# Optimization experiments

Hardware: AMD Instinct MI355X
Metric: run time of the kernel (lower is better)

## Reference

```python
import jax, jax.numpy as jnp
import numpy as np

N = 100000
E = 1600000
D = 128


def setup_inputs() -> dict:
    key = jax.random.key(0)
    ks = jax.random.split(key, 8)
    x = jax.random.normal(ks[0], (N, D), dtype=jnp.float32)
    edge_index = jax.random.randint(ks[1], (2, E), 0, N, dtype=jnp.int64)
    # Xavier-uniform linear weights, zero-ish biases (PyTorch default bias is uniform; keep small random)
    def xavier(k, fan_in, fan_out):
        limit = float(np.sqrt(6.0 / (fan_in + fan_out)))
        return jax.random.uniform(k, (fan_out, fan_in), minval=-limit, maxval=limit, dtype=jnp.float32)
    W1 = xavier(ks[2], D, D); b1 = jnp.zeros((D,), jnp.float32)
    W2 = xavier(ks[3], D, D); b2 = jnp.zeros((D,), jnp.float32)
    W3 = xavier(ks[4], D, D); b3 = jnp.zeros((D,), jnp.float32)
    return {"x": x, "edge_index": edge_index, "W1": W1, "b1": b1,
            "W2": W2, "b2": b2, "W3": W3, "b3": b3}


def reference(x, edge_index, W1, b1, W2, b2, W3, b3):
    n = x.shape[0]
    loop = jnp.arange(n, dtype=edge_index.dtype)
    row = jnp.concatenate([edge_index[0], loop])  # source (x_j index)
    col = jnp.concatenate([edge_index[1], loop])  # target (aggregation index)
    # degree over row after self-loops; every node appears at least once
    deg = jax.ops.segment_sum(jnp.ones_like(row, dtype=x.dtype), row, num_segments=n)
    dis = deg ** -0.5
    norm = dis[row] * dis[col]  # [E+N]

    def gconv(h, W, b):
        h = h @ W.T + b                      # linear projection [N, D]
        msg = norm[:, None] * h[row]         # gather + elementwise norm [E+N, D]
        return jax.ops.segment_sum(msg, col, num_segments=n)  # scatter-add

    h = jax.nn.relu(gconv(x, W1, b1))
    h = jax.nn.relu(gconv(h, W2, b2))
    h = jax.nn.relu(gconv(h, W3, b3))
    return h
```

## Files before the change

### kernel.cpp

```cpp
#include <hip/hip_runtime.h>
#include <hip/hip_fp16.h>

#define THREADS 256
#define ELL 64

typedef _Float16 f16x8 __attribute__((ext_vector_type(8)));
typedef float f32x4 __attribute__((ext_vector_type(4)));

__device__ inline uint2 pack_half4(float4 v) {
    __half2 a = __floats2half2_rn(v.x, v.y);
    __half2 b = __floats2half2_rn(v.z, v.w);
    uint2 o;
    o.x = *reinterpret_cast<unsigned int*>(&a);
    o.y = *reinterpret_cast<unsigned int*>(&b);
    return o;
}
__device__ inline float4 unpack_half4(uint2 v) {
    __half2 a = *reinterpret_cast<__half2*>(&v.x);
    __half2 b = *reinterpret_cast<__half2*>(&v.y);
    float2 f0 = __half22float2(a);
    float2 f1 = __half22float2(b);
    return make_float4(f0.x, f0.y, f1.x, f1.y);
}


__global__ void detect_kernel(const int* __restrict__ ei, int* __restrict__ flag) {
    if (blockIdx.x == 0 && threadIdx.x == 0) {
        int nz = 0;
        for (int i = 1; i < 256; i += 2) nz |= ei[i];
        *flag = (nz == 0) ? 1 : 0;
    }
}

__global__ void preinit_kernel(int* __restrict__ deg, int* __restrict__ fill,
                               int* __restrict__ csr, int n) {
    int i = blockIdx.x * blockDim.x + threadIdx.x;
    if (i < n) {
        deg[i] = 1;
        fill[i] = 1;
        csr[(size_t)i * ELL] = i;
    }
}

__global__ void edge_kernel(const int* __restrict__ ei, const int* __restrict__ flag,
                            int* __restrict__ deg, int* __restrict__ fill,
                            int* __restrict__ csr, int eN) {
    int e = blockIdx.x * blockDim.x + threadIdx.x;
    if (e >= eN) return;
    int r, c;
    if (*flag) {
        const long long* e64 = (const long long*)ei;
        r = (int)e64[e];
        c = (int)e64[eN + e];
    } else {
        r = ei[e];
        c = ei[eN + e];
    }
    atomicAdd(&deg[r], 1);
    int pos = atomicAdd(&fill[c], 1);
    csr[(size_t)c * ELL + pos] = r;
}

__global__ void dis_kernel(const int* __restrict__ deg, float* __restrict__ dis, int n) {
    int i = blockIdx.x * blockDim.x + threadIdx.x;
    if (i < n) dis[i] = 1.0f / sqrtf((float)deg[i]);
}

__global__ void sumw_kernel(const int* __restrict__ csr, const int* __restrict__ fill,
                            const float* __restrict__ dis, float* __restrict__ sumw, int n) {
    int i = blockIdx.x * blockDim.x + threadIdx.x;
    if (i >= n) return;
    int len = fill[i];
    const int base = i * ELL;
    float t = 0.f;
    for (int j = 0; j < len; ++j) t += dis[csr[base + j]];
    sumw[i] = dis[i] * t;
}

__global__ void tofp16_kernel(const float4* __restrict__ x, uint2* __restrict__ o, int total) {
    int i = blockIdx.x * blockDim.x + threadIdx.x;
    if (i < total) o[i] = pack_half4(x[i]);
}

__global__ void wfrag_kernel(const float* __restrict__ w0, const float* __restrict__ w1,
                             const float* __restrict__ w2, _Float16* __restrict__ wf) {
    int i = blockIdx.x * blockDim.x + threadIdx.x;
    if (i >= 3 * 8 * 4 * 64) return;
    int lane = i & 63;
    int kt = (i >> 6) & 3;
    int nt = (i >> 8) & 7;
    int l  = i >> 11;
    const float* w = (l == 0) ? w0 : (l == 1) ? w1 : w2;
    int o  = nt * 16 + (lane & 15);
    int kb = kt * 32 + (lane >> 4) * 8;
    _Float16* dst = wf + (size_t)i * 8;
#pragma unroll
    for (int j = 0; j < 8; ++j) dst[j] = (_Float16)w[o * 128 + kb + j];
}


__global__ void agg_kernel(const uint2* __restrict__ h, const int* __restrict__ csr,
                           const int* __restrict__ fill, const float* __restrict__ dis,
                           uint2* __restrict__ out, int n) {
    const int wid = blockIdx.x * (blockDim.x >> 6) + (threadIdx.x >> 6);
    const int lane = threadIdx.x & 63;
    const int half = lane >> 5;
    const int l32 = lane & 31;
    if (wid >= n) return;
    const int len = fill[wid];
    const int base = wid * ELL;

    float4 a0 = make_float4(0.f, 0.f, 0.f, 0.f);
    float4 a1 = make_float4(0.f, 0.f, 0.f, 0.f);
    int j = half;
    for (; j + 2 < len; j += 4) {
        int u0 = csr[base + j];
        int u1 = csr[base + j + 2];
        float w0 = dis[u0];
        float w1 = dis[u1];
        float4 v0 = unpack_half4(h[(size_t)u0 * 32 + l32]);
        float4 v1 = unpack_half4(h[(size_t)u1 * 32 + l32]);
        a0.x = fmaf(w0, v0.x, a0.x); a0.y = fmaf(w0, v0.y, a0.y);
        a0.z = fmaf(w0, v0.z, a0.z); a0.w = fmaf(w0, v0.w, a0.w);
        a1.x = fmaf(w1, v1.x, a1.x); a1.y = fmaf(w1, v1.y, a1.y);
        a1.z = fmaf(w1, v1.z, a1.z); a1.w = fmaf(w1, v1.w, a1.w);
    }
    if (j < len) {
        int u = csr[base + j];
        float w = dis[u];
        float4 v = unpack_half4(h[(size_t)u * 32 + l32]);
        a0.x = fmaf(w, v.x, a0.x); a0.y = fmaf(w, v.y, a0.y);
        a0.z = fmaf(w, v.z, a0.z); a0.w = fmaf(w, v.w, a0.w);
    }
    a0.x += a1.x; a0.y += a1.y; a0.z += a1.z; a0.w += a1.w;

    a0.x += __shfl_xor(a0.x, 32, 64);
    a0.y += __shfl_xor(a0.y, 32, 64);
    a0.z += __shfl_xor(a0.z, 32, 64);
    a0.w += __shfl_xor(a0.w, 32, 64);

    if (half == 0) {
        const float dg = dis[wid];
        a0.x *= dg; a0.y *= dg; a0.z *= dg; a0.w *= dg;
        out[(size_t)wid * 32 + l32] = pack_half4(a0);
    }
}

template <bool OUT16>
__global__ __launch_bounds__(THREADS) void lin_mfma_kernel(
    const _Float16* __restrict__ a16, const _Float16* __restrict__ wfrag,
    const float* __restrict__ bias, const float* __restrict__ sumw,
    float* __restrict__ outf, _Float16* __restrict__ outh, int n) {
    const int lane = threadIdx.x & 63;
    const int g = lane >> 4;
    const int m15 = lane & 15;
    const int wavesPerBlock = blockDim.x >> 6;
    const int wave = blockIdx.x * wavesPerBlock + (threadIdx.x >> 6);
    const int nwaves = gridDim.x * wavesPerBlock;

    f16x8 wf[8][4];
#pragma unroll
    for (int nt = 0; nt < 8; ++nt)
#pragma unroll
        for (int kt = 0; kt < 4; ++kt)
            wf[nt][kt] = *reinterpret_cast<const f16x8*>(
                wfrag + ((size_t)((nt * 4 + kt) * 64 + lane)) * 8);

    const int ntiles = (n + 15) >> 4;
    for (int t = wave; t < ntiles; t += nwaves) {
        const int myrow = t * 16 + m15;
        const int rr = (myrow < n) ? myrow : (n - 1);
        const _Float16* arow = a16 + (size_t)rr * 128 + g * 8;
        f16x8 af[4];
#pragma unroll
        for (int kt = 0; kt < 4; ++kt)
            af[kt] = *reinterpret_cast<const f16x8*>(arow + kt * 32);

        f32x4 acc[8];
#pragma unroll
        for (int nt = 0; nt < 8; ++nt) acc[nt] = (f32x4){0.f, 0.f, 0.f, 0.f};
#pragma unroll
        for (int kt = 0; kt < 4; ++kt)
#pragma unroll
            for (int nt = 0; nt < 8; ++nt)
                acc[nt] = __builtin_amdgcn_mfma_f32_16x16x32_f16(
                    wf[nt][kt], af[kt], acc[nt], 0, 0, 0);

        if (myrow < n) {
            const float sw = sumw[myrow];
#pragma unroll
            for (int nt = 0; nt < 8; ++nt) {
                const float4 b4 = *reinterpret_cast<const float4*>(bias + nt * 16 + g * 4);
                float vx = fmaxf(acc[nt][0] + sw * b4.x, 0.f);
                float vy = fmaxf(acc[nt][1] + sw * b4.y, 0.f);
                float vz = fmaxf(acc[nt][2] + sw * b4.z, 0.f);
                float vw = fmaxf(acc[nt][3] + sw * b4.w, 0.f);
                size_t oidx = (size_t)myrow * 128 + nt * 16 + g * 4;
                if (OUT16) {
                    *reinterpret_cast<uint2*>(outh + oidx) =
                        pack_half4(make_float4(vx, vy, vz, vw));
                } else {
                    *reinterpret_cast<float4*>(outf + oidx) =
                        make_float4(vx, vy, vz, vw);
                }
            }
        }
    }
}


extern "C" void kernel_launch(void* const* d_in, const int* in_sizes, int n_in,
                              void* d_out, int out_size, void* d_ws, size_t ws_size,
                              hipStream_t stream) {
    const float* x  = (const float*)d_in[0];
    const int*   ei = (const int*)d_in[1];
    const float* Ws[3] = {(const float*)d_in[2], (const float*)d_in[4], (const float*)d_in[6]};
    const float* bs[3] = {(const float*)d_in[3], (const float*)d_in[5], (const float*)d_in[7]};
    const int n = in_sizes[0] / 128;
    const int e = in_sizes[1] / 2;

    char* ws = (char*)d_ws;
    size_t cur = 0;
    auto alloc = [&](size_t bytes) {
        void* p = ws + cur;
        cur = (cur + bytes + 255) & ~(size_t)255;
        return p;
    };
    uint2*     A16  = (uint2*)alloc((size_t)n * 128 * 2);
    uint2*     H16  = (uint2*)alloc((size_t)n * 128 * 2);
    int*       csr  = (int*)  alloc((size_t)n * ELL * 4);
    int*       deg  = (int*)  alloc((size_t)n * 4);
    int*       fill = (int*)  alloc((size_t)n * 4);
    float*     dis  = (float*)alloc((size_t)n * 4);
    float*     sumw = (float*)alloc((size_t)n * 4);
    _Float16*  wf   = (_Float16*)alloc(3 * 8 * 4 * 64 * 8 * 2);
    int*       flag = (int*)  alloc(4);

    detect_kernel<<<1, 64, 0, stream>>>(ei, flag);
    preinit_kernel<<<(n + 255) / 256, 256, 0, stream>>>(deg, fill, csr, n);
    edge_kernel<<<(e + 255) / 256, 256, 0, stream>>>(ei, flag, deg, fill, csr, e);
    dis_kernel<<<(n + 255) / 256, 256, 0, stream>>>(deg, dis, n);
    sumw_kernel<<<(n + 255) / 256, 256, 0, stream>>>(csr, fill, dis, sumw, n);
    tofp16_kernel<<<(n * 32 + 255) / 256, 256, 0, stream>>>((const float4*)x, H16, n * 32);
    wfrag_kernel<<<(6144 + 255) / 256, 256, 0, stream>>>(Ws[0], Ws[1], Ws[2], wf);

    for (int l = 0; l < 3; ++l) {
        agg_kernel<<<(n + 3) / 4, 256, 0, stream>>>(
            H16, csr, fill, dis, A16, n);
        const _Float16* wfl = wf + (size_t)l * 8 * 4 * 64 * 8;
        if (l < 2) {
            lin_mfma_kernel<true><<<512, THREADS, 0, stream>>>(
                (const _Float16*)A16, wfl, bs[l], sumw,
                nullptr, (_Float16*)H16, n);
        } else {
            lin_mfma_kernel<false><<<512, THREADS, 0, stream>>>(
                (const _Float16*)A16, wfl, bs[l], sumw,
                (float*)d_out, nullptr, n);
        }
    }
}
```

Baseline: 477.3 us.

## Precompute per-edge normalized weights and batch edges per thread in CSR build

The sumw kernel now writes a per-slot edge weight array (dis[i]*dis[u]) in the ELL layout, and the aggregation kernel reads it contiguously instead of doing a dependent random gather of dis[u] and a final scale by dis[i]. The edge kernel also processes four edges per thread to issue more independent loads and atomics per thread. This trades an extra n*64*4-byte weight buffer and a write pass in sumw for fewer random accesses in each of the three aggregation passes.

New measurement: 482.3 us. No clear change (+1.0%).

```diff
diff --git a/kernel.cpp b/kernel.cpp
--- a/kernel.cpp
+++ b/kernel.cpp
@@ -3,6 +3,7 @@
 
 #define THREADS 256
 #define ELL 64
+#define EPT 4
 
 typedef _Float16 f16x8 __attribute__((ext_vector_type(8)));
 typedef float f32x4 __attribute__((ext_vector_type(4)));
@@ -45,20 +46,33 @@
 __global__ void edge_kernel(const int* __restrict__ ei, const int* __restrict__ flag,
                             int* __restrict__ deg, int* __restrict__ fill,
                             int* __restrict__ csr, int eN) {
-    int e = blockIdx.x * blockDim.x + threadIdx.x;
-    if (e >= eN) return;
-    int r, c;
+    const int t = blockIdx.x * blockDim.x + threadIdx.x;
+    const int base = t * EPT;
+    if (base >= eN) return;
+    int r[EPT], c[EPT];
+    const int m = min(EPT, eN - base);
     if (*flag) {
         const long long* e64 = (const long long*)ei;
-        r = (int)e64[e];
-        c = (int)e64[eN + e];
+#pragma unroll
+        for (int k = 0; k < EPT; ++k) {
+            if (k < m) { r[k] = (int)e64[base + k]; c[k] = (int)e64[eN + base + k]; }
+        }
     } else {
-        r = ei[e];
-        c = ei[eN + e];
-    }
-    atomicAdd(&deg[r], 1);
-    int pos = atomicAdd(&fill[c], 1);
-    csr[(size_t)c * ELL + pos] = r;
+#pragma unroll
+        for (int k = 0; k < EPT; ++k) {
+            if (k < m) { r[k] = ei[base + k]; c[k] = ei[eN + base + k]; }
+        }
+    }
+#pragma unroll
+    for (int k = 0; k < EPT; ++k)
+        if (k < m) atomicAdd(&deg[r[k]], 1);
+    int pos[EPT];
+#pragma unroll
+    for (int k = 0; k < EPT; ++k)
+        if (k < m) pos[k] = atomicAdd(&fill[c[k]], 1);
+#pragma unroll
+    for (int k = 0; k < EPT; ++k)
+        if (k < m) csr[(size_t)c[k] * ELL + pos[k]] = r[k];
 }
 
 __global__ void dis_kernel(const int* __restrict__ deg, float* __restrict__ dis, int n) {
@@ -67,14 +81,20 @@
 }
 
 __global__ void sumw_kernel(const int* __restrict__ csr, const int* __restrict__ fill,
-                            const float* __restrict__ dis, float* __restrict__ sumw, int n) {
+                            const float* __restrict__ dis, float* __restrict__ sumw,
+                            float* __restrict__ w32, int n) {
     int i = blockIdx.x * blockDim.x + threadIdx.x;
     if (i >= n) return;
     int len = fill[i];
     const int base = i * ELL;
+    const float dg = dis[i];
     float t = 0.f;
-    for (int j = 0; j < len; ++j) t += dis[csr[base + j]];
-    sumw[i] = dis[i] * t;
+    for (int j = 0; j < len; ++j) {
+        float w = dg * dis[csr[base + j]];
+        w32[base + j] = w;
+        t += w;
+    }
+    sumw[i] = t;
 }
 
 __global__ void tofp16_kernel(const float4* __restrict__ x, uint2* __restrict__ o, int total) {
@@ -100,7 +120,7 @@
 
 
 __global__ void agg_kernel(const uint2* __restrict__ h, const int* __restrict__ csr,
-                           const int* __restrict__ fill, const float* __restrict__ dis,
+                           const int* __restrict__ fill, const float* __restrict__ w32,
                            uint2* __restrict__ out, int n) {
     const int wid = blockIdx.x * (blockDim.x >> 6) + (threadIdx.x >> 6);
     const int lane = threadIdx.x & 63;
@@ -116,8 +136,8 @@
     for (; j + 2 < len; j += 4) {
         int u0 = csr[base + j];
         int u1 = csr[base + j + 2];
-        float w0 = dis[u0];
-        float w1 = dis[u1];
+        float w0 = w32[base + j];
+        float w1 = w32[base + j + 2];
         float4 v0 = unpack_half4(h[(size_t)u0 * 32 + l32]);
         float4 v1 = unpack_half4(h[(size_t)u1 * 32 + l32]);
         a0.x = fmaf(w0, v0.x, a0.x); a0.y = fmaf(w0, v0.y, a0.y);
@@ -127,7 +147,7 @@
     }
     if (j < len) {
         int u = csr[base + j];
-        float w = dis[u];
+        float w = w32[base + j];
         float4 v = unpack_half4(h[(size_t)u * 32 + l32]);
         a0.x = fmaf(w, v.x, a0.x); a0.y = fmaf(w, v.y, a0.y);
         a0.z = fmaf(w, v.z, a0.z); a0.w = fmaf(w, v.w, a0.w);
@@ -140,8 +160,6 @@
     a0.w += __shfl_xor(a0.w, 32, 64);
 
     if (half == 0) {
-        const float dg = dis[wid];
-        a0.x *= dg; a0.y *= dg; a0.z *= dg; a0.w *= dg;
         out[(size_t)wid * 32 + l32] = pack_half4(a0);
     }
 }
@@ -229,6 +247,7 @@
     uint2*     A16  = (uint2*)alloc((size_t)n * 128 * 2);
     uint2*     H16  = (uint2*)alloc((size_t)n * 128 * 2);
     int*       csr  = (int*)  alloc((size_t)n * ELL * 4);
+    float*     w32  = (float*)alloc((size_t)n * ELL * 4);
     int*       deg  = (int*)  alloc((size_t)n * 4);
     int*       fill = (int*)  alloc((size_t)n * 4);
     float*     dis  = (float*)alloc((size_t)n * 4);
@@ -238,15 +257,16 @@
 
     detect_kernel<<<1, 64, 0, stream>>>(ei, flag);
     preinit_kernel<<<(n + 255) / 256, 256, 0, stream>>>(deg, fill, csr, n);
-    edge_kernel<<<(e + 255) / 256, 256, 0, stream>>>(ei, flag, deg, fill, csr, e);
+    edge_kernel<<<((e + EPT - 1) / EPT + 255) / 256, 256, 0, stream>>>(
+        ei, flag, deg, fill, csr, e);
     dis_kernel<<<(n + 255) / 256, 256, 0, stream>>>(deg, dis, n);
-    sumw_kernel<<<(n + 255) / 256, 256, 0, stream>>>(csr, fill, dis, sumw, n);
+    sumw_kernel<<<(n + 255) / 256, 256, 0, stream>>>(csr, fill, dis, sumw, w32, n);
     tofp16_kernel<<<(n * 32 + 255) / 256, 256, 0, stream>>>((const float4*)x, H16, n * 32);
     wfrag_kernel<<<(6144 + 255) / 256, 256, 0, stream>>>(Ws[0], Ws[1], Ws[2], wf);
 
     for (int l = 0; l < 3; ++l) {
         agg_kernel<<<(n + 3) / 4, 256, 0, stream>>>(
-            H16, csr, fill, dis, A16, n);
+            H16, csr, fill, w32, A16, n);
         const _Float16* wfl = wf + (size_t)l * 8 * 4 * 64 * 8;
         if (l < 2) {
             lin_mfma_kernel<true><<<512, THREADS, 0, stream>>>(
```
